# Performance work log

Measured on AMD Instinct MI355X. Metric: run time of the kernel, lower is better.

## Reference

```python
import jax, jax.numpy as jnp
import numpy as np

NUM_HEADS = 8


def _forward(x, Wq, bq, Wk, bk, Wv, bv, Wo, bo, w1, b1, w2, b2, tau):
    B, S, E = x.shape
    H = NUM_HEADS
    hd = E // H
    scale = hd ** -0.5

    def heads(t):
        return t.reshape(B, S, H, hd).transpose(0, 2, 1, 3)  # [B,H,S,hd]

    q = heads(x @ Wq + bq)
    k = heads(x @ Wk + bk)
    v = heads(x @ Wv + bv)
    s = jnp.einsum('bhqd,bhkd->bhqk', q, k) * scale  # [B,H,S,S]

    # ---- autopoietic transform (vectorized over batch, no mask) ----
    s = jnp.clip(jnp.nan_to_num(s, nan=0.0, posinf=10.0, neginf=-10.0), -15.0, 15.0)
    ma = s.mean(axis=1)  # mean over heads -> [B,S,S]
    eps_safe = 0.05  # clamp(eps=1e-6, 0.05, 0.8)
    sa = jnp.clip(jnp.clip(ma, -8.0, 8.0) * eps_safe, -10.0, 10.0)
    # 1x1 conv on [1,1,S,S] == per-channel scalar scale+bias -> [B,C,S,S]
    hid = jax.nn.relu(jnp.clip(sa[:, None] * w1[None, :, None, None]
                               + b1[None, :, None, None], -5.0, 5.0))
    ap = jnp.clip(jnp.einsum('bcij,c->bij', hid, w2) + b2, -5.0, 5.0)
    taylor = jnp.clip(1.0 + 0.05 * (ap * 50.0), 0.5, 1.5)
    sig = jax.nn.sigmoid(taylor)
    p = jax.nn.softmax(jnp.clip(ma, -10.0, 10.0), axis=-1)
    Hent = -p * jnp.log(p + 1e-6)
    Fm = jax.nn.softmax(3.0 * Hent, axis=-1)
    t = sig * Fm
    eo = jnp.sqrt((ma * ma).sum(axis=(1, 2), keepdims=True)) + 1e-4  # fro norm
    et = jnp.sqrt((t * t).sum(axis=(1, 2), keepdims=True)) + 1e-4
    t = jnp.clip(eo / et, 0.8, 1.2) * t
    tm = t.mean(axis=(1, 2), keepdims=True)
    om = ma.mean(axis=(1, 2), keepdims=True)
    tstd = jnp.sqrt(jnp.clip(((t - tm) ** 2).mean(axis=(1, 2), keepdims=True), 0.01, None))
    ostd = jnp.sqrt(jnp.clip(((ma - om) ** 2).mean(axis=(1, 2), keepdims=True), 0.01, None))
    gd = jnp.clip(ostd / tstd, 0.8, 1.2)
    ar = jnp.clip(jnp.abs(ma).max(axis=(1, 2), keepdims=True), 1.0, 10.0)
    sm = jnp.clip(0.3 / jnp.log1p(ar), 0.1, 0.5)
    st = tm + sm * gd * (t - tm)  # scaled_transform
    ent = Hent.mean(axis=(1, 2), keepdims=True)
    ne = ent / jnp.log(jnp.float32(S))  # normalized entropy (max_entropy = log S)
    rr = 0.4 * (1.0 - jnp.clip(ne, 0.0, 0.4))  # residual ratio (base 0.4, entropy-damped)
    # blend transform back into per-head scores (res_scale = 1.0)
    s = s + rr[:, None] * (st - ma)[:, None]

    attn = jax.nn.softmax(s / tau, axis=-1)
    out = jnp.einsum('bhqk,bhkd->bhqd', attn, v)
    out = out.transpose(0, 2, 1, 3).reshape(B, S, E)
    return out @ Wo + bo


def setup_inputs() -> dict:
    key = jax.random.key(0)
    ks = jax.random.split(key, 8)
    B, S, E, C = 4, 512, 512, 128
    w_scale = 0.02
    return {
        'x': jax.random.normal(ks[0], (B, S, E), dtype=jnp.float32),
        'Wq': jax.random.normal(ks[1], (E, E), dtype=jnp.float32) * w_scale,
        'bq': jnp.zeros((E,), jnp.float32),
        'Wk': jax.random.normal(ks[2], (E, E), dtype=jnp.float32) * w_scale,
        'bk': jnp.zeros((E,), jnp.float32),
        'Wv': jax.random.normal(ks[3], (E, E), dtype=jnp.float32) * w_scale,
        'bv': jnp.zeros((E,), jnp.float32),
        'Wo': jax.random.normal(ks[4], (E, E), dtype=jnp.float32) * w_scale,
        'bo': jnp.zeros((E,), jnp.float32),
        'w1': jax.random.normal(ks[5], (C,), dtype=jnp.float32) * 0.5,
        'b1': jnp.zeros((C,), jnp.float32),
        'w2': jax.random.normal(ks[6], (C,), dtype=jnp.float32) * 0.1,
        'b2': jnp.zeros((1,), jnp.float32),
        'tau': jnp.ones((1,), jnp.float32),
    }


def reference(x, Wq, bq, Wk, bk, Wv, bv, Wo, bo, w1, b1, w2, b2, tau):
    return _forward(x, Wq, bq, Wk, bk, Wv, bv, Wo, bo, w1, b1, w2, b2, tau)
```

## Files before the change

### kernel.cpp

```cpp
#include <hip/hip_runtime.h>
#include <math.h>

#define BB 4
#define SS 512
#define EE 512
#define NH 8
#define HD 64
#define NC 128
#define NTAB 4096

typedef _Float16 f16x8 __attribute__((ext_vector_type(8)));
typedef float f32x4 __attribute__((ext_vector_type(4)));

struct HL { _Float16 h, l; };

__device__ __forceinline__ float clampf(float v, float lo, float hi) {
  return fminf(fmaxf(v, lo), hi);
}
__device__ __forceinline__ HL split16(float x) {
  HL r;
  r.h = (_Float16)x;
  r.l = (_Float16)(x - (float)r.h);
  return r;
}

__device__ __forceinline__ float waveRedSum(float v) {
#pragma unroll
  for (int o = 32; o; o >>= 1) v += __shfl_xor(v, o);
  return v;
}
__device__ __forceinline__ float waveRedMax(float v) {
#pragma unroll
  for (int o = 32; o; o >>= 1) v = fmaxf(v, __shfl_xor(v, o));
  return v;
}
__device__ __forceinline__ float blockRedSum(float v, float* red) {
  int tid = threadIdx.x;
  v = waveRedSum(v);
  __syncthreads();
  if ((tid & 63) == 0) red[tid >> 6] = v;
  __syncthreads();
  return red[0] + red[1] + red[2] + red[3];
}
__device__ __forceinline__ float blockRedMax(float v, float* red) {
  int tid = threadIdx.x;
  v = waveRedMax(v);
  __syncthreads();
  if ((tid & 63) == 0) red[tid >> 6] = v;
  __syncthreads();
  return fmaxf(fmaxf(red[0], red[1]), fmaxf(red[2], red[3]));
}

__global__ __launch_bounds__(256) void k_prep(
    const float* __restrict__ w1, const float* __restrict__ b1,
    const float* __restrict__ w2, const float* __restrict__ b2,
    float* __restrict__ T, const float* __restrict__ x,
    _Float16* __restrict__ xh, _Float16* __restrict__ xl,
    const float* __restrict__ Wq, const float* __restrict__ Wk,
    const float* __restrict__ Wv, const float* __restrict__ Wo,
    _Float16* __restrict__ Wth, _Float16* __restrict__ Wtl) {
  const int bid = blockIdx.x;
  const int tid = threadIdx.x;
  if (bid < 17) {
    int idx = bid * 256 + tid;
    if (idx > NTAB) return;
    float sa = -0.4f + (float)idx * (0.8f / (float)NTAB);
    float ap = 0.f;
#pragma unroll 4
    for (int c = 0; c < NC; ++c) {
      float h = fminf(fmaxf(sa * w1[c] + b1[c], 0.f), 5.f);
      ap += h * w2[c];
    }
    ap = clampf(ap + b2[0], -5.f, 5.f);
    float tay = clampf(1.0f + 0.05f * (ap * 50.0f), 0.5f, 1.5f);
    T[idx] = 1.0f / (1.0f + expf(-tay));
  } else if (bid < 529) {
    int idx = ((bid - 17) * 256 + tid) * 8;
    float4 u0 = *(const float4*)(x + idx);
    float4 u1 = *(const float4*)(x + idx + 4);
    float f[8] = {u0.x, u0.y, u0.z, u0.w, u1.x, u1.y, u1.z, u1.w};
    f16x8 h, l;
#pragma unroll
    for (int j = 0; j < 8; ++j) {
      HL r = split16(f[j]);
      h[j] = r.h;
      l[j] = r.l;
    }
    *(f16x8*)(xh + idx) = h;
    *(f16x8*)(xl + idx) = l;
  } else {
    const int j = bid - 529;
    const int z = j >> 6;
    const int rem = j & 63;
    const int k0 = (rem & 7) * 64, n0 = (rem >> 3) * 64;
    const float* W = (z == 0) ? Wq : (z == 1) ? Wk : (z == 2) ? Wv : Wo;
    __shared__ float Tt[64][68];
    const int r = tid >> 2, c = (tid & 3) * 16;
#pragma unroll
    for (int jj = 0; jj < 16; jj += 4)
      *(float4*)&Tt[r][c + jj] =
          *(const float4*)(W + (size_t)(k0 + r) * EE + n0 + c + jj);
    __syncthreads();
    f16x8 h0, l0, h1, l1;
#pragma unroll
    for (int jj = 0; jj < 8; ++jj) {
      HL r0 = split16(Tt[c + jj][r]);
      HL r1 = split16(Tt[c + 8 + jj][r]);
      h0[jj] = r0.h; l0[jj] = r0.l;
      h1[jj] = r1.h; l1[jj] = r1.l;
    }
    _Float16* dh = Wth + ((size_t)z * EE + n0 + r) * EE + k0 + c;
    _Float16* dl = Wtl + ((size_t)z * EE + n0 + r) * EE + k0 + c;
    *(f16x8*)dh = h0;
    *(f16x8*)(dh + 8) = h1;
    *(f16x8*)dl = l0;
    *(f16x8*)(dl + 8) = l1;
  }
}

__global__ __launch_bounds__(256) void k_qkv_mfma(
    const _Float16* __restrict__ xh, const _Float16* __restrict__ xl,
    const _Float16* __restrict__ Wth, const _Float16* __restrict__ Wtl,
    const float* __restrict__ bq, const float* __restrict__ bk,
    const float* __restrict__ bv,
    _Float16* __restrict__ qh, _Float16* __restrict__ ql,
    _Float16* __restrict__ kh, _Float16* __restrict__ kl,
    _Float16* __restrict__ vth, _Float16* __restrict__ vtl) {
  const int which = blockIdx.z;
  const int tid = threadIdx.x;
  const int wave = tid >> 6, lane = tid & 63;
  const int quad = lane >> 4, l16 = lane & 15;
  const int m0 = blockIdx.y * 64;
  const int n0 = blockIdx.x * 64;
  const _Float16* Bh = Wth + (size_t)which * EE * EE;
  const _Float16* Bl = Wtl + (size_t)which * EE * EE;

  __shared__ __align__(16) char smpool[36864];
  _Float16(*LAh)[72] = (_Float16(*)[72])(smpool);
  _Float16(*LAl)[72] = (_Float16(*)[72])(smpool + 9216);
  _Float16(*LBh)[72] = (_Float16(*)[72])(smpool + 18432);
  _Float16(*LBl)[72] = (_Float16(*)[72])(smpool + 27648);
  float(*TR)[68] = (float(*)[68])(smpool);

  const int sr0 = tid >> 3, sc0 = (tid & 7) * 8;
  const int sr1 = (tid + 256) >> 3, sc1 = sc0;

  f32x4 acc[4] = {};
  for (int k0 = 0; k0 < EE; k0 += 64) {
    if (k0) __syncthreads();
    *(f16x8*)&LAh[sr0][sc0] = *(const f16x8*)(xh + (size_t)(m0 + sr0) * EE + k0 + sc0);
    *(f16x8*)&LAl[sr0][sc0] = *(const f16x8*)(xl + (size_t)(m0 + sr0) * EE + k0 + sc0);
    *(f16x8*)&LBh[sr0][sc0] = *(const f16x8*)(Bh + (size_t)(n0 + sr0) * EE + k0 + sc0);
    *(f16x8*)&LBl[sr0][sc0] = *(const f16x8*)(Bl + (size_t)(n0 + sr0) * EE + k0 + sc0);
    *(f16x8*)&LAh[sr1][sc1] = *(const f16x8*)(xh + (size_t)(m0 + sr1) * EE + k0 + sc1);
    *(f16x8*)&LAl[sr1][sc1] = *(const f16x8*)(xl + (size_t)(m0 + sr1) * EE + k0 + sc1);
    *(f16x8*)&LBh[sr1][sc1] = *(const f16x8*)(Bh + (size_t)(n0 + sr1) * EE + k0 + sc1);
    *(f16x8*)&LBl[sr1][sc1] = *(const f16x8*)(Bl + (size_t)(n0 + sr1) * EE + k0 + sc1);
    __syncthreads();
#pragma unroll
    for (int kk = 0; kk < 64; kk += 32) {
      f16x8 ah = *(const f16x8*)&LAh[wave * 16 + l16][kk + quad * 8];
      f16x8 al = *(const f16x8*)&LAl[wave * 16 + l16][kk + quad * 8];
#pragma unroll
      for (int nt = 0; nt < 4; ++nt) {
        f16x8 bhf = *(const f16x8*)&LBh[nt * 16 + l16][kk + quad * 8];
        f16x8 blf = *(const f16x8*)&LBl[nt * 16 + l16][kk + quad * 8];
        acc[nt] = __builtin_amdgcn_mfma_f32_16x16x32_f16(ah, bhf, acc[nt], 0, 0, 0);
        acc[nt] = __builtin_amdgcn_mfma_f32_16x16x32_f16(ah, blf, acc[nt], 0, 0, 0);
        acc[nt] = __builtin_amdgcn_mfma_f32_16x16x32_f16(al, bhf, acc[nt], 0, 0, 0);
      }
    }
  }
  const float* bias = (which == 0) ? bq : (which == 1) ? bk : bv;
  if (which == 2) {
    __syncthreads();
#pragma unroll
    for (int nt = 0; nt < 4; ++nt) {
      const int dcol = nt * 16 + l16;
      const float bb = bias[n0 + nt * 16 + l16];
#pragma unroll
      for (int r = 0; r < 4; ++r)
        TR[dcol][wave * 16 + quad * 4 + r] = acc[nt][r] + bb;
    }
    __syncthreads();
    const int d = tid >> 2, cc = (tid & 3) * 16;
    const int bh = (m0 >> 9) * NH + (n0 >> 6);
    const int si0 = m0 & 511;
    f16x8 h0, l0, h1, l1;
#pragma unroll
    for (int jj = 0; jj < 8; ++jj) {
      HL r0 = split16(TR[d][cc + jj]);
      HL r1 = split16(TR[d][cc + 8 + jj]);
      h0[jj] = r0.h; l0[jj] = r0.l;
      h1[jj] = r1.h; l1[jj] = r1.l;
    }
    _Float16* dh = vth + ((size_t)bh * HD + d) * SS + si0 + cc;
    _Float16* dl = vtl + ((size_t)bh * HD + d) * SS + si0 + cc;
    *(f16x8*)dh = h0;
    *(f16x8*)(dh + 8) = h1;
    *(f16x8*)dl = l0;
    *(f16x8*)(dl + 8) = l1;
  } else {
    const float postscale = (which == 0) ? 0.125f : 1.0f;
    const int mbase = m0 + wave * 16 + quad * 4;
#pragma unroll
    for (int nt = 0; nt < 4; ++nt) {
      const int col = n0 + nt * 16 + l16;
      const float bb = bias[col];
      const int hh = col >> 6, d = col & 63;
#pragma unroll
      for (int r = 0; r < 4; ++r) {
        const int mm = mbase + r;
        const int b_ = mm >> 9, si = mm & 511;
        const size_t idx = (((size_t)(b_ * NH + hh)) * SS + si) * HD + d;
        const float val = (acc[nt][r] + bb) * postscale;
        HL sp = split16(val);
        (which ? kh : qh)[idx] = sp.h;
        (which ? kl : ql)[idx] = sp.l;
      }
    }
  }
}

__global__ __launch_bounds__(256) void k_scores_mfma(
    const _Float16* __restrict__ qh, const _Float16* __restrict__ ql,
    const _Float16* __restrict__ kh, const _Float16* __restrict__ kl,
    float* __restrict__ s) {
  const int bh = blockIdx.z;
  const int i0 = blockIdx.y * 64, j0 = blockIdx.x * 64;
  const int tid = threadIdx.x;
  const int wave = tid >> 6, lane = tid & 63;
  const int quad = lane >> 4, l16 = lane & 15;

  __shared__ _Float16 Qh[64][72], Ql[64][72], Kh[64][72], Kl[64][72];
  const int r = tid >> 2, c = (tid & 3) * 16;
  {
    const size_t qoff = ((size_t)bh * SS + i0 + r) * HD + c;
    const size_t koff = ((size_t)bh * SS + j0 + r) * HD + c;
    *(f16x8*)&Qh[r][c] = *(const f16x8*)(qh + qoff);
    *(f16x8*)&Qh[r][c + 8] = *(const f16x8*)(qh + qoff + 8);
    *(f16x8*)&Ql[r][c] = *(const f16x8*)(ql + qoff);
    *(f16x8*)&Ql[r][c + 8] = *(const f16x8*)(ql + qoff + 8);
    *(f16x8*)&Kh[r][c] = *(const f16x8*)(kh + koff);
    *(f16x8*)&Kh[r][c + 8] = *(const f16x8*)(kh + koff + 8);
    *(f16x8*)&Kl[r][c] = *(const f16x8*)(kl + koff);
    *(f16x8*)&Kl[r][c + 8] = *(const f16x8*)(kl + koff + 8);
  }
  __syncthreads();

  f16x8 a_hi[2], a_lo[2];
#pragma unroll
  for (int ks = 0; ks < 2; ++ks) {
    a_hi[ks] = *(const f16x8*)&Qh[wave * 16 + l16][ks * 32 + quad * 8];
    a_lo[ks] = *(const f16x8*)&Ql[wave * 16 + l16][ks * 32 + quad * 8];
  }
  f32x4 acc[4] = {};
#pragma unroll
  for (int ks = 0; ks < 2; ++ks) {
#pragma unroll
    for (int t = 0; t < 4; ++t) {
      f16x8 b_hi = *(const f16x8*)&Kh[t * 16 + l16][ks * 32 + quad * 8];
      f16x8 b_lo = *(const f16x8*)&Kl[t * 16 + l16][ks * 32 + quad * 8];
      acc[t] = __builtin_amdgcn_mfma_f32_16x16x32_f16(a_hi[ks], b_hi,
                                                      acc[t], 0, 0, 0);
      acc[t] = __builtin_amdgcn_mfma_f32_16x16x32_f16(a_hi[ks], b_lo,
                                                      acc[t], 0, 0, 0);
      acc[t] = __builtin_amdgcn_mfma_f32_16x16x32_f16(a_lo[ks], b_hi,
                                                      acc[t], 0, 0, 0);
    }
  }
  float* sb = s + (size_t)bh * SS * SS;
#pragma unroll
  for (int t = 0; t < 4; ++t) {
#pragma unroll
    for (int r2 = 0; r2 < 4; ++r2) {
      float val = clampf(acc[t][r2], -15.0f, 15.0f);
      sb[(size_t)(i0 + wave * 16 + quad * 4 + r2) * SS + j0 + t * 16 + l16] = val;
    }
  }
}

__global__ __launch_bounds__(64) void k_rowstat(
    const float* __restrict__ s, const float* __restrict__ T,
    float* __restrict__ ma, float* __restrict__ t_un,
    float* __restrict__ rowred) {
  const int row = blockIdx.x;
  const int b_ = row >> 9, i = row & 511;
  const int lane = threadIdx.x;

  float4 a0 = {0.f, 0.f, 0.f, 0.f}, a1 = {0.f, 0.f, 0.f, 0.f};
#pragma unroll
  for (int hh = 0; hh < NH; ++hh) {
    const float4* p = reinterpret_cast<const float4*>(
                          s + (((size_t)(b_ * NH + hh) * SS) + i) * SS) +
                      lane * 2;
    float4 u0 = p[0], u1 = p[1];
    a0.x += u0.x; a0.y += u0.y; a0.z += u0.z; a0.w += u0.w;
    a1.x += u1.x; a1.y += u1.y; a1.z += u1.z; a1.w += u1.w;
  }
  float m[8] = {a0.x * 0.125f, a0.y * 0.125f, a0.z * 0.125f, a0.w * 0.125f,
                a1.x * 0.125f, a1.y * 0.125f, a1.z * 0.125f, a1.w * 0.125f};
  {
    float4* mp = reinterpret_cast<float4*>(ma + ((size_t)b_ * SS + i) * SS) +
                 lane * 2;
    float4 w0 = {m[0], m[1], m[2], m[3]}, w1v = {m[4], m[5], m[6], m[7]};
    mp[0] = w0;
    mp[1] = w1v;
  }
  float sma = 0.f, sma2 = 0.f, mabs = 0.f;
#pragma unroll
  for (int e = 0; e < 8; ++e) {
    sma += m[e];
    sma2 += m[e] * m[e];
    mabs = fmaxf(mabs, fabsf(m[e]));
  }
  sma = waveRedSum(sma);
  sma2 = waveRedSum(sma2);
  mabs = waveRedMax(mabs);

  float ex[8], esum = 0.f;
#pragma unroll
  for (int e = 0; e < 8; ++e) {
    ex[e] = expf(clampf(m[e], -10.f, 10.f));
    esum += ex[e];
  }
  esum = waveRedSum(esum);
  float inv = 1.0f / esum;
  float Hv[8], sH = 0.f;
#pragma unroll
  for (int e = 0; e < 8; ++e) {
    float p = ex[e] * inv;
    Hv[e] = -p * logf(p + 1e-6f);
    sH += Hv[e];
  }
  sH = waveRedSum(sH);

  float fx[8], fsum = 0.f;
#pragma unroll
  for (int e = 0; e < 8; ++e) {
    fx[e] = expf(3.0f * Hv[e]);
    fsum += fx[e];
  }
  fsum = waveRedSum(fsum);
  float finv = 1.0f / fsum;

  float t[8], st = 0.f, st2 = 0.f;
#pragma unroll
  for (int e = 0; e < 8; ++e) {
    float sa = clampf(m[e], -8.f, 8.f) * 0.05f;
    float pos = (sa + 0.4f) * ((float)NTAB / 0.8f);
    int idx = (int)pos;
    idx = idx < 0 ? 0 : (idx > NTAB - 1 ? NTAB - 1 : idx);
    float frac = pos - (float)idx;
    float g0 = T[idx], g1 = T[idx + 1];
    float sig = g0 + (g1 - g0) * frac;
    t[e] = sig * fx[e] * finv;
    st += t[e];
    st2 += t[e] * t[e];
  }
  st = waveRedSum(st);
  st2 = waveRedSum(st2);
  {
    float4* tp = reinterpret_cast<float4*>(t_un + ((size_t)b_ * SS + i) * SS) +
                 lane * 2;
    float4 w0 = {t[0], t[1], t[2], t[3]}, w1v = {t[4], t[5], t[6], t[7]};
    tp[0] = w0;
    tp[1] = w1v;
  }
  if (lane == 0) {
    float* rp = rowred + (size_t)row * 8;
    rp[0] = sma; rp[1] = sma2; rp[2] = mabs;
    rp[3] = st;  rp[4] = st2;  rp[5] = sH;
  }
}

__global__ __launch_bounds__(256) void k_consts(
    const float* __restrict__ rowred, float* __restrict__ cst) {
  const int b_ = blockIdx.x;
  const int tid = threadIdx.x;
  __shared__ float red[4];
  const float* r0 = rowred + ((size_t)b_ * SS + tid * 2) * 8;
  const float* r1 = r0 + 8;
  float sma = blockRedSum(r0[0] + r1[0], red);
  float sma2 = blockRedSum(r0[1] + r1[1], red);
  float mabs = blockRedMax(fmaxf(r0[2], r1[2]), red);
  float st = blockRedSum(r0[3] + r1[3], red);
  float st2 = blockRedSum(r0[4] + r1[4], red);
  float sH = blockRedSum(r0[5] + r1[5], red);
  if (tid == 0) {
    const float N = (float)(SS * SS);
    float eo = sqrtf(sma2) + 1e-4f;
    float et = sqrtf(st2) + 1e-4f;
    float r = clampf(eo / et, 0.8f, 1.2f);
    float tmean = r * st / N;
    float om = sma / N;
    float vart = r * r * fmaxf(st2 / N - (st / N) * (st / N), 0.f);
    float tstd = sqrtf(fmaxf(vart, 0.01f));
    float varo = fmaxf(sma2 / N - om * om, 0.f);
    float ostd = sqrtf(fmaxf(varo, 0.01f));
    float gd = clampf(ostd / tstd, 0.8f, 1.2f);
    float ar = clampf(mabs, 1.f, 10.f);
    float sm = clampf(0.3f / log1pf(ar), 0.1f, 0.5f);
    float ent = sH / N;
    float ne = ent / logf((float)SS);
    float rr = 0.4f * (1.f - clampf(ne, 0.f, 0.4f));
    float G = sm * gd;
    cst[b_ * 4 + 0] = rr * (1.f - G) * tmean;
    cst[b_ * 4 + 1] = rr * G * r;
    cst[b_ * 4 + 2] = rr;
  }
}

__global__ __launch_bounds__(256) void k_av_fused(
    const float* __restrict__ s, const float* __restrict__ ma,
    const float* __restrict__ t_un, const float* __restrict__ cst,
    const float* __restrict__ tau, const _Float16* __restrict__ vth,
    const _Float16* __restrict__ vtl, _Float16* __restrict__ oh,
    _Float16* __restrict__ ol) {
  const int bh = blockIdx.y;
  const int b_ = bh >> 3, hh = bh & 7;
  const int m0 = blockIdx.x * 64;
  const int tid = threadIdx.x;
  const int wave = tid >> 6, lane = tid & 63;
  const int quad = lane >> 4, l16 = lane & 15;

  const float c0 = cst[b_ * 4 + 0], c1 = cst[b_ * 4 + 1], c2 = cst[b_ * 4 + 2];
  const float itau = 1.0f / tau[0];

  __shared__ _Float16 Ph[64][40], Pl[64][40];
  __shared__ float Zp[64][4];

  const int srow = tid >> 2;
  const int ci = tid & 3;
  const int schunk = ci * 8;
  const size_t sbase = ((size_t)bh * SS + m0 + srow) * SS + schunk;
  const size_t mbase = ((size_t)b_ * SS + m0 + srow) * SS + schunk;

  float4 sv0 = *(const float4*)(s + sbase);
  float4 sv1 = *(const float4*)(s + sbase + 4);
  float4 mv0 = *(const float4*)(ma + mbase);
  float4 mv1 = *(const float4*)(ma + mbase + 4);
  float4 tv0 = *(const float4*)(t_un + mbase);
  float4 tv1 = *(const float4*)(t_un + mbase + 4);

  float zpart = 0.f;
  f32x4 acc[4] = {};
  for (int k0 = 0; k0 < SS; k0 += 32) {
    if (k0) __syncthreads();
    {
      float svv[8] = {sv0.x, sv0.y, sv0.z, sv0.w, sv1.x, sv1.y, sv1.z, sv1.w};
      float mvv[8] = {mv0.x, mv0.y, mv0.z, mv0.w, mv1.x, mv1.y, mv1.z, mv1.w};
      float tvv[8] = {tv0.x, tv0.y, tv0.z, tv0.w, tv1.x, tv1.y, tv1.z, tv1.w};
      f16x8 hv, lv;
#pragma unroll
      for (int j = 0; j < 8; ++j) {
        float vv = (svv[j] + c0 + c1 * tvv[j] - c2 * mvv[j]) * itau;
        float e = expf(vv) * 1.52587890625e-05f;
        zpart += e;
        HL r = split16(e);
        hv[j] = r.h;
        lv[j] = r.l;
      }
      *(f16x8*)&Ph[srow][schunk] = hv;
      *(f16x8*)&Pl[srow][schunk] = lv;
    }
    __syncthreads();
    if (k0 + 32 < SS) {
      sv0 = *(const float4*)(s + sbase + k0 + 32);
      sv1 = *(const float4*)(s + sbase + k0 + 36);
      mv0 = *(const float4*)(ma + mbase + k0 + 32);
      mv1 = *(const float4*)(ma + mbase + k0 + 36);
      tv0 = *(const float4*)(t_un + mbase + k0 + 32);
      tv1 = *(const float4*)(t_un + mbase + k0 + 36);
    }
    const size_t boff = ((size_t)bh * HD + wave * 16 + l16) * SS + k0 + quad * 8;
    f16x8 bh_ = *(const f16x8*)(vth + boff);
    f16x8 bl_ = *(const f16x8*)(vtl + boff);
#pragma unroll
    for (int mt = 0; mt < 4; ++mt) {
      f16x8 ah = *(const f16x8*)&Ph[mt * 16 + l16][quad * 8];
      f16x8 al = *(const f16x8*)&Pl[mt * 16 + l16][quad * 8];
      acc[mt] = __builtin_amdgcn_mfma_f32_16x16x32_f16(ah, bh_, acc[mt], 0, 0, 0);
      acc[mt] = __builtin_amdgcn_mfma_f32_16x16x32_f16(ah, bl_, acc[mt], 0, 0, 0);
      acc[mt] = __builtin_amdgcn_mfma_f32_16x16x32_f16(al, bh_, acc[mt], 0, 0, 0);
    }
  }
  __syncthreads();
  Zp[srow][ci] = zpart;
  __syncthreads();
#pragma unroll
  for (int mt = 0; mt < 4; ++mt) {
#pragma unroll
    for (int r = 0; r < 4; ++r) {
      const int lr = mt * 16 + quad * 4 + r;
      const float Z = Zp[lr][0] + Zp[lr][1] + Zp[lr][2] + Zp[lr][3];
      const float oV = acc[mt][r] / Z;
      const int si = m0 + lr;
      const size_t idx =
          ((size_t)(b_ * SS + si)) * EE + hh * HD + wave * 16 + l16;
      HL sp = split16(oV);
      oh[idx] = sp.h;
      ol[idx] = sp.l;
    }
  }
}

__global__ __launch_bounds__(256) void k_out_mfma(
    const _Float16* __restrict__ oh, const _Float16* __restrict__ ol,
    const _Float16* __restrict__ Wth, const _Float16* __restrict__ Wtl,
    const float* __restrict__ bo, float* __restrict__ out) {
  const int tid = threadIdx.x;
  const int wave = tid >> 6, lane = tid & 63;
  const int quad = lane >> 4, l16 = lane & 15;
  const int m0 = blockIdx.y * 64;
  const int n0 = blockIdx.x * 64;
  const _Float16* Bh = Wth + (size_t)3 * EE * EE;
  const _Float16* Bl = Wtl + (size_t)3 * EE * EE;

  __shared__ _Float16 LAh[64][72], LAl[64][72], LBh[64][72], LBl[64][72];

  const int sr0 = tid >> 3, sc0 = (tid & 7) * 8;
  const int sr1 = (tid + 256) >> 3, sc1 = sc0;

  f32x4 acc[4] = {};
  for (int k0 = 0; k0 < EE; k0 += 64) {
    if (k0) __syncthreads();
    *(f16x8*)&LAh[sr0][sc0] = *(const f16x8*)(oh + (size_t)(m0 + sr0) * EE + k0 + sc0);
    *(f16x8*)&LAl[sr0][sc0] = *(const f16x8*)(ol + (size_t)(m0 + sr0) * EE + k0 + sc0);
    *(f16x8*)&LBh[sr0][sc0] = *(const f16x8*)(Bh + (size_t)(n0 + sr0) * EE + k0 + sc0);
    *(f16x8*)&LBl[sr0][sc0] = *(const f16x8*)(Bl + (size_t)(n0 + sr0) * EE + k0 + sc0);
    *(f16x8*)&LAh[sr1][sc1] = *(const f16x8*)(oh + (size_t)(m0 + sr1) * EE + k0 + sc1);
    *(f16x8*)&LAl[sr1][sc1] = *(const f16x8*)(ol + (size_t)(m0 + sr1) * EE + k0 + sc1);
    *(f16x8*)&LBh[sr1][sc1] = *(const f16x8*)(Bh + (size_t)(n0 + sr1) * EE + k0 + sc1);
    *(f16x8*)&LBl[sr1][sc1] = *(const f16x8*)(Bl + (size_t)(n0 + sr1) * EE + k0 + sc1);
    __syncthreads();
#pragma unroll
    for (int kk = 0; kk < 64; kk += 32) {
      f16x8 ah = *(const f16x8*)&LAh[wave * 16 + l16][kk + quad * 8];
      f16x8 al = *(const f16x8*)&LAl[wave * 16 + l16][kk + quad * 8];
#pragma unroll
      for (int nt = 0; nt < 4; ++nt) {
        f16x8 bhf = *(const f16x8*)&LBh[nt * 16 + l16][kk + quad * 8];
        f16x8 blf = *(const f16x8*)&LBl[nt * 16 + l16][kk + quad * 8];
        acc[nt] = __builtin_amdgcn_mfma_f32_16x16x32_f16(ah, bhf, acc[nt], 0, 0, 0);
        acc[nt] = __builtin_amdgcn_mfma_f32_16x16x32_f16(ah, blf, acc[nt], 0, 0, 0);
        acc[nt] = __builtin_amdgcn_mfma_f32_16x16x32_f16(al, bhf, acc[nt], 0, 0, 0);
      }
    }
  }
  const int mbase = m0 + wave * 16 + quad * 4;
#pragma unroll
  for (int nt = 0; nt < 4; ++nt) {
    const int col = n0 + nt * 16 + l16;
    const float bb = bo[col];
#pragma unroll
    for (int r = 0; r < 4; ++r) {
      const int m = mbase + r;
      out[(size_t)m * EE + col] = acc[nt][r] + bb;
    }
  }
}

extern "C" void kernel_launch(void* const* d_in, const int* in_sizes, int n_in,
                              void* d_out, int out_size, void* d_ws,
                              size_t ws_size, hipStream_t stream) {
  const float* x = (const float*)d_in[0];
  const float* Wq = (const float*)d_in[1];
  const float* bq = (const float*)d_in[2];
  const float* Wk = (const float*)d_in[3];
  const float* bk = (const float*)d_in[4];
  const float* Wv = (const float*)d_in[5];
  const float* bv = (const float*)d_in[6];
  const float* Wo = (const float*)d_in[7];
  const float* bo = (const float*)d_in[8];
  const float* w1 = (const float*)d_in[9];
  const float* b1 = (const float*)d_in[10];
  const float* w2 = (const float*)d_in[11];
  const float* b2 = (const float*)d_in[12];
  const float* tau = (const float*)d_in[13];
  float* out = (float*)d_out;

  const size_t NX = (size_t)2048 * EE;
  const size_t NW = (size_t)4 * EE * EE;
  const size_t NQK = (size_t)BB * NH * SS * HD;
  const size_t NS = (size_t)BB * NH * SS * SS;

  _Float16* xh = (_Float16*)d_ws;
  _Float16* xl = xh + NX;
  _Float16* Wth = xl + NX;
  _Float16* Wtl = Wth + NW;
  _Float16* qh = Wtl + NW;
  _Float16* ql = qh + NQK;
  _Float16* kh = ql + NQK;
  _Float16* kl = kh + NQK;
  _Float16* vth = kl + NQK;
  _Float16* vtl = vth + NQK;
  float* s = (float*)(vtl + NQK);
  float* ma = s + NS;
  float* t_un = ma + (size_t)BB * SS * SS;
  float* T = t_un + (size_t)BB * SS * SS;
  float* rowred = T + 8192;
  float* cst = rowred + 2048 * 8;
  _Float16* oh = xh;
  _Float16* ol = xl;

  k_prep<<<785, 256, 0, stream>>>(w1, b1, w2, b2, T, x, xh, xl, Wq, Wk, Wv, Wo,
                                  Wth, Wtl);
  k_qkv_mfma<<<dim3(8, 32, 3), 256, 0, stream>>>(xh, xl, Wth, Wtl, bq, bk, bv,
                                                 qh, ql, kh, kl, vth, vtl);
  k_scores_mfma<<<dim3(8, 8, 32), 256, 0, stream>>>(qh, ql, kh, kl, s);
  k_rowstat<<<2048, 64, 0, stream>>>(s, T, ma, t_un, rowred);
  k_consts<<<4, 256, 0, stream>>>(rowred, cst);
  k_av_fused<<<dim3(8, 32), 256, 0, stream>>>(s, ma, t_un, cst, tau, vth, vtl,
                                              oh, ol);
  k_out_mfma<<<dim3(8, 32), 256, 0, stream>>>(oh, ol, Wth, Wtl, bo, out);
}
```

Baseline: 170.5 us.

## Register-prefetch GEMM tiles and halve AV row tile to double grid size

The QKV and output-projection GEMMs now load the next K-slice of the A and B tiles into registers while MFMAs run on the current shared-memory tile, overlapping global-load latency with compute. The fused attention-times-V kernel now uses 32-row tiles instead of 64, doubling the grid from 256 to 512 blocks so more of the GPU's compute units are busy. Only half the threads stage the probability tile, and V fragments are re-read twice as often across blocks. The prefetch raises register pressure in the GEMMs.

```diff
diff --git a/kernel.cpp b/kernel.cpp
--- a/kernel.cpp
+++ b/kernel.cpp
@@ -143,20 +143,40 @@
   float(*TR)[68] = (float(*)[68])(smpool);
 
   const int sr0 = tid >> 3, sc0 = (tid & 7) * 8;
-  const int sr1 = (tid + 256) >> 3, sc1 = sc0;
+  const int sr1 = sr0 + 32;
+
+  f16x8 rA0h = *(const f16x8*)(xh + (size_t)(m0 + sr0) * EE + sc0);
+  f16x8 rA0l = *(const f16x8*)(xl + (size_t)(m0 + sr0) * EE + sc0);
+  f16x8 rB0h = *(const f16x8*)(Bh + (size_t)(n0 + sr0) * EE + sc0);
+  f16x8 rB0l = *(const f16x8*)(Bl + (size_t)(n0 + sr0) * EE + sc0);
+  f16x8 rA1h = *(const f16x8*)(xh + (size_t)(m0 + sr1) * EE + sc0);
+  f16x8 rA1l = *(const f16x8*)(xl + (size_t)(m0 + sr1) * EE + sc0);
+  f16x8 rB1h = *(const f16x8*)(Bh + (size_t)(n0 + sr1) * EE + sc0);
+  f16x8 rB1l = *(const f16x8*)(Bl + (size_t)(n0 + sr1) * EE + sc0);
 
   f32x4 acc[4] = {};
   for (int k0 = 0; k0 < EE; k0 += 64) {
     if (k0) __syncthreads();
-    *(f16x8*)&LAh[sr0][sc0] = *(const f16x8*)(xh + (size_t)(m0 + sr0) * EE + k0 + sc0);
-    *(f16x8*)&LAl[sr0][sc0] = *(const f16x8*)(xl + (size_t)(m0 + sr0) * EE + k0 + sc0);
-    *(f16x8*)&LBh[sr0][sc0] = *(const f16x8*)(Bh + (size_t)(n0 + sr0) * EE + k0 + sc0);
-    *(f16x8*)&LBl[sr0][sc0] = *(const f16x8*)(Bl + (size_t)(n0 + sr0) * EE + k0 + sc0);
-    *(f16x8*)&LAh[sr1][sc1] = *(const f16x8*)(xh + (size_t)(m0 + sr1) * EE + k0 + sc1);
-    *(f16x8*)&LAl[sr1][sc1] = *(const f16x8*)(xl + (size_t)(m0 + sr1) * EE + k0 + sc1);
-    *(f16x8*)&LBh[sr1][sc1] = *(const f16x8*)(Bh + (size_t)(n0 + sr1) * EE + k0 + sc1);
-    *(f16x8*)&LBl[sr1][sc1] = *(const f16x8*)(Bl + (size_t)(n0 + sr1) * EE + k0 + sc1);
+    *(f16x8*)&LAh[sr0][sc0] = rA0h;
+    *(f16x8*)&LAl[sr0][sc0] = rA0l;
+    *(f16x8*)&LBh[sr0][sc0] = rB0h;
+    *(f16x8*)&LBl[sr0][sc0] = rB0l;
+    *(f16x8*)&LAh[sr1][sc0] = rA1h;
+    *(f16x8*)&LAl[sr1][sc0] = rA1l;
+    *(f16x8*)&LBh[sr1][sc0] = rB1h;
+    *(f16x8*)&LBl[sr1][sc0] = rB1l;
     __syncthreads();
+    if (k0 + 64 < EE) {
+      const int kn = k0 + 64;
+      rA0h = *(const f16x8*)(xh + (size_t)(m0 + sr0) * EE + kn + sc0);
+      rA0l = *(const f16x8*)(xl + (size_t)(m0 + sr0) * EE + kn + sc0);
+      rB0h = *(const f16x8*)(Bh + (size_t)(n0 + sr0) * EE + kn + sc0);
+      rB0l = *(const f16x8*)(Bl + (size_t)(n0 + sr0) * EE + kn + sc0);
+      rA1h = *(const f16x8*)(xh + (size_t)(m0 + sr1) * EE + kn + sc0);
+      rA1l = *(const f16x8*)(xl + (size_t)(m0 + sr1) * EE + kn + sc0);
+      rB1h = *(const f16x8*)(Bh + (size_t)(n0 + sr1) * EE + kn + sc0);
+      rB1l = *(const f16x8*)(Bl + (size_t)(n0 + sr1) * EE + kn + sc0);
+    }
 #pragma unroll
     for (int kk = 0; kk < 64; kk += 32) {
       f16x8 ah = *(const f16x8*)&LAh[wave * 16 + l16][kk + quad * 8];
@@ -419,7 +439,7 @@
     _Float16* __restrict__ ol) {
   const int bh = blockIdx.y;
   const int b_ = bh >> 3, hh = bh & 7;
-  const int m0 = blockIdx.x * 64;
+  const int m0 = blockIdx.x * 32;
   const int tid = threadIdx.x;
   const int wave = tid >> 6, lane = tid & 63;
   const int quad = lane >> 4, l16 = lane & 15;
@@ -427,27 +447,31 @@
   const float c0 = cst[b_ * 4 + 0], c1 = cst[b_ * 4 + 1], c2 = cst[b_ * 4 + 2];
   const float itau = 1.0f / tau[0];
 
-  __shared__ _Float16 Ph[64][40], Pl[64][40];
-  __shared__ float Zp[64][4];
-
+  __shared__ _Float16 Ph[32][40], Pl[32][40];
+  __shared__ float Zp[32][4];
+
+  const bool stager = (tid < 128);
   const int srow = tid >> 2;
   const int ci = tid & 3;
   const int schunk = ci * 8;
-  const size_t sbase = ((size_t)bh * SS + m0 + srow) * SS + schunk;
-  const size_t mbase = ((size_t)b_ * SS + m0 + srow) * SS + schunk;
-
-  float4 sv0 = *(const float4*)(s + sbase);
-  float4 sv1 = *(const float4*)(s + sbase + 4);
-  float4 mv0 = *(const float4*)(ma + mbase);
-  float4 mv1 = *(const float4*)(ma + mbase + 4);
-  float4 tv0 = *(const float4*)(t_un + mbase);
-  float4 tv1 = *(const float4*)(t_un + mbase + 4);
+  const size_t sbase = ((size_t)bh * SS + m0 + (srow & 31)) * SS + schunk;
+  const size_t mbase = ((size_t)b_ * SS + m0 + (srow & 31)) * SS + schunk;
+
+  float4 sv0, sv1, mv0, mv1, tv0, tv1;
+  if (stager) {
+    sv0 = *(const float4*)(s + sbase);
+    sv1 = *(const float4*)(s + sbase + 4);
+    mv0 = *(const float4*)(ma + mbase);
+    mv1 = *(const float4*)(ma + mbase + 4);
+    tv0 = *(const float4*)(t_un + mbase);
+    tv1 = *(const float4*)(t_un + mbase + 4);
+  }
 
   float zpart = 0.f;
-  f32x4 acc[4] = {};
+  f32x4 acc[2] = {};
   for (int k0 = 0; k0 < SS; k0 += 32) {
     if (k0) __syncthreads();
-    {
+    if (stager) {
       float svv[8] = {sv0.x, sv0.y, sv0.z, sv0.w, sv1.x, sv1.y, sv1.z, sv1.w};
       float mvv[8] = {mv0.x, mv0.y, mv0.z, mv0.w, mv1.x, mv1.y, mv1.z, mv1.w};
       float tvv[8] = {tv0.x, tv0.y, tv0.z, tv0.w, tv1.x, tv1.y, tv1.z, tv1.w};
@@ -465,7 +489,7 @@
       *(f16x8*)&Pl[srow][schunk] = lv;
     }
     __syncthreads();
-    if (k0 + 32 < SS) {
+    if (stager && k0 + 32 < SS) {
       sv0 = *(const float4*)(s + sbase + k0 + 32);
       sv1 = *(const float4*)(s + sbase + k0 + 36);
       mv0 = *(const float4*)(ma + mbase + k0 + 32);
@@ -477,7 +501,7 @@
     f16x8 bh_ = *(const f16x8*)(vth + boff);
     f16x8 bl_ = *(const f16x8*)(vtl + boff);
 #pragma unroll
-    for (int mt = 0; mt < 4; ++mt) {
+    for (int mt = 0; mt < 2; ++mt) {
       f16x8 ah = *(const f16x8*)&Ph[mt * 16 + l16][quad * 8];
       f16x8 al = *(const f16x8*)&Pl[mt * 16 + l16][quad * 8];
       acc[mt] = __builtin_amdgcn_mfma_f32_16x16x32_f16(ah, bh_, acc[mt], 0, 0, 0);
@@ -486,10 +510,10 @@
     }
   }
   __syncthreads();
-  Zp[srow][ci] = zpart;
+  if (stager) Zp[srow][ci] = zpart;
   __syncthreads();
 #pragma unroll
-  for (int mt = 0; mt < 4; ++mt) {
+  for (int mt = 0; mt < 2; ++mt) {
 #pragma unroll
     for (int r = 0; r < 4; ++r) {
       const int lr = mt * 16 + quad * 4 + r;
@@ -520,20 +544,40 @@
   __shared__ _Float16 LAh[64][72], LAl[64][72], LBh[64][72], LBl[64][72];
 
   const int sr0 = tid >> 3, sc0 = (tid & 7) * 8;
-  const int sr1 = (tid + 256) >> 3, sc1 = sc0;
+  const int sr1 = sr0 + 32;
+
+  f16x8 rA0h = *(const f16x8*)(oh + (size_t)(m0 + sr0) * EE + sc0);
+  f16x8 rA0l = *(const f16x8*)(ol + (size_t)(m0 + sr0) * EE + sc0);
+  f16x8 rB0h = *(const f16x8*)(Bh + (size_t)(n0 + sr0) * EE + sc0);
+  f16x8 rB0l = *(const f16x8*)(Bl + (size_t)(n0 + sr0) * EE + sc0);
+  f16x8 rA1h = *(const f16x8*)(oh + (size_t)(m0 + sr1) * EE + sc0);
+  f16x8 rA1l = *(const f16x8*)(ol + (size_t)(m0 + sr1) * EE + sc0);
+  f16x8 rB1h = *(const f16x8*)(Bh + (size_t)(n0 + sr1) * EE + sc0);
+  f16x8 rB1l = *(const f16x8*)(Bl + (size_t)(n0 + sr1) * EE + sc0);
 
   f32x4 acc[4] = {};
   for (int k0 = 0; k0 < EE; k0 += 64) {
     if (k0) __syncthreads();
-    *(f16x8*)&LAh[sr0][sc0] = *(const f16x8*)(oh + (size_t)(m0 + sr0) * EE + k0 + sc0);
-    *(f16x8*)&LAl[sr0][sc0] = *(const f16x8*)(ol + (size_t)(m0 + sr0) * EE + k0 + sc0);
-    *(f16x8*)&LBh[sr0][sc0] = *(const f16x8*)(Bh + (size_t)(n0 + sr0) * EE + k0 + sc0);
-    *(f16x8*)&LBl[sr0][sc0] = *(const f16x8*)(Bl + (size_t)(n0 + sr0) * EE + k0 + sc0);
-    *(f16x8*)&LAh[sr1][sc1] = *(const f16x8*)(oh + (size_t)(m0 + sr1) * EE + k0 + sc1);
-    *(f16x8*)&LAl[sr1][sc1] = *(const f16x8*)(ol + (size_t)(m0 + sr1) * EE + k0 + sc1);
-    *(f16x8*)&LBh[sr1][sc1] = *(const f16x8*)(Bh + (size_t)(n0 + sr1) * EE + k0 + sc1);
-    *(f16x8*)&LBl[sr1][sc1] = *(const f16x8*)(Bl + (size_t)(n0 + sr1) * EE + k0 + sc1);
+    *(f16x8*)&LAh[sr0][sc0] = rA0h;
+    *(f16x8*)&LAl[sr0][sc0] = rA0l;
+    *(f16x8*)&LBh[sr0][sc0] = rB0h;
+    *(f16x8*)&LBl[sr0][sc0] = rB0l;
+    *(f16x8*)&LAh[sr1][sc0] = rA1h;
+    *(f16x8*)&LAl[sr1][sc0] = rA1l;
+    *(f16x8*)&LBh[sr1][sc0] = rB1h;
+    *(f16x8*)&LBl[sr1][sc0] = rB1l;
     __syncthreads();
+    if (k0 + 64 < EE) {
+      const int kn = k0 + 64;
+      rA0h = *(const f16x8*)(oh + (size_t)(m0 + sr0) * EE + kn + sc0);
+      rA0l = *(const f16x8*)(ol + (size_t)(m0 + sr0) * EE + kn + sc0);
+      rB0h = *(const f16x8*)(Bh + (size_t)(n0 + sr0) * EE + kn + sc0);
+      rB0l = *(const f16x8*)(Bl + (size_t)(n0 + sr0) * EE + kn + sc0);
+      rA1h = *(const f16x8*)(oh + (size_t)(m0 + sr1) * EE + kn + sc0);
+      rA1l = *(const f16x8*)(ol + (size_t)(m0 + sr1) * EE + kn + sc0);
+      rB1h = *(const f16x8*)(Bh + (size_t)(n0 + sr1) * EE + kn + sc0);
+      rB1l = *(const f16x8*)(Bl + (size_t)(n0 + sr1) * EE + kn + sc0);
+    }
 #pragma unroll
     for (int kk = 0; kk < 64; kk += 32) {
       f16x8 ah = *(const f16x8*)&LAh[wave * 16 + l16][kk + quad * 8];
@@ -611,7 +655,7 @@
   k_scores_mfma<<<dim3(8, 8, 32), 256, 0, stream>>>(qh, ql, kh, kl, s);
   k_rowstat<<<2048, 64, 0, stream>>>(s, T, ma, t_un, rowred);
   k_consts<<<4, 256, 0, stream>>>(rowred, cst);
-  k_av_fused<<<dim3(8, 32), 256, 0, stream>>>(s, ma, t_un, cst, tau, vth, vtl,
-                                              oh, ol);
+  k_av_fused<<<dim3(16, 32), 256, 0, stream>>>(s, ma, t_un, cst, tau, vth, vtl,
+                                               oh, ol);
   k_out_mfma<<<dim3(8, 32), 256, 0, stream>>>(oh, ol, Wth, Wtl, bo, out);
 }
```

Result: no change. 167.4 us (-1.8%).
